# Optimization experiments

Hardware: AMD Instinct MI355X
Metric: run time of the kernel (lower is better)

The kernel has to match this reference:

```python
import jax, jax.numpy as jnp
import numpy as np
from jax import lax


def _gauss1d(size, sigma):
    k = np.arange(size, dtype=np.float32) - (size - 1) / 2.0
    k = np.exp(-0.5 * (k / sigma) ** 2)
    return k / k.sum()


def _make_kernel(scale, sigma):
    # make_odd
    kx, ky, kz = [s + 1 if s % 2 == 0 else s for s in scale]
    kH = _gauss1d(kx, sigma)
    kW = _gauss1d(ky, sigma)
    kD = _gauss1d(kz, sigma)
    kern = kH[:, None, None] * kW[None, :, None] * kD[None, None, :]  # (kx, ky, kz)
    kern = np.transpose(kern, (2, 0, 1))  # permute(2,0,1) -> (kz, kx, ky)
    return jnp.asarray(kern, dtype=jnp.float32)


def setup_inputs() -> dict:
    key = jax.random.key(0)
    x = jax.random.normal(key, (2, 1, 256, 256, 256), dtype=jnp.float32)
    kernel0 = _make_kernel((2, 2, 2), 1.0)  # (3,3,3)
    kernel1 = _make_kernel((4, 4, 4), 1.0)  # (5,5,5)
    return {"x": x, "kernel0": kernel0, "kernel1": kernel1}


def _blur_down(x, kernel, stride):
    # replicate pad by k//2 per spatial dim, then depthwise (C=1) conv3d.
    pad = [(0, 0), (0, 0)] + [(k // 2, k // 2) for k in kernel.shape]
    xp = jnp.pad(x, pad, mode='edge')
    # strided VALID conv == full blur followed by [::s] slicing (output ceil(H/s))
    return lax.conv_general_dilated(
        xp, kernel[None, None].astype(x.dtype),
        window_strides=stride, padding='VALID',
        dimension_numbers=('NCDHW', 'OIDHW', 'NCDHW'))


def reference(x, kernel0, kernel1):
    d1 = _blur_down(x, kernel0, (2, 2, 2))  # (2,1,128,128,128)
    d2 = _blur_down(x, kernel1, (4, 4, 4))  # (2,1,64,64,64)
    return (x, d1, d2)
```

## Files before the change

kernel.cpp:

```cpp
#include <hip/hip_runtime.h>

#define S_IN 256
#define S_D1 128
#define S_D2 64
#define IN_PER_BATCH (S_IN * S_IN * S_IN)
#define D1_PER_BATCH (S_D1 * S_D1 * S_D1)
#define D2_PER_BATCH (S_D2 * S_D2 * S_D2)
#define X_ELEMS (2 * IN_PER_BATCH)
#define D1_ELEMS (2 * D1_PER_BATCH)
#define D2_ELEMS (2 * D2_PER_BATCH)

#define TD 8
#define TH 8
#define TW 32
#define LZ 12
#define LY 12
#define LX 40
#define NV (LZ * LY * (LX / 4))
#define LDS_ELEMS (LZ * LY * LX)

__global__ __launch_bounds__(256) void fused_pyramid(
    const float* __restrict__ x, const float* __restrict__ k0,
    const float* __restrict__ k1, float* __restrict__ out0,
    float* __restrict__ out1, float* __restrict__ out2)
{
    __shared__ float ls[LDS_ELEMS];
    __shared__ float kw0[27];
    __shared__ float kw1[125];

    const int tid = threadIdx.x;
    if (tid < 27) kw0[tid] = k0[tid];
    else if (tid >= 32 && tid < 157) kw1[tid - 32] = k1[tid - 32];

    const int bx = blockIdx.x;
    const int lin = (bx & 7) * 2048 + (bx >> 3);
    const int wt = lin & 7;
    const int hy = (lin >> 3) & 31;
    const int dz = (lin >> 8) & 31;
    const int n  = lin >> 13;

    const int x0 = wt * TW;
    const int y0 = hy * TH;
    const int z0 = dz * TD;

    const float* xb = x + (size_t)n * IN_PER_BATCH;
    float* ob0 = out0 + (size_t)n * IN_PER_BATCH;
    float* ob1 = out1 + (size_t)n * D1_PER_BATCH;
    float* ob2 = out2 + (size_t)n * D2_PER_BATCH;

    float4 vals[6];
#pragma unroll
    for (int i = 0; i < 6; ++i) {
        int v = tid + (i << 8);
        if (v < NV) {
            int row = v / 10;
            int j   = v - row * 10;
            int lz  = row / LY;
            int ly  = row - lz * LY;
            int gz = z0 + lz - 2; gz = gz < 0 ? 0 : (gz > 255 ? 255 : gz);
            int gy = y0 + ly - 2; gy = gy < 0 ? 0 : (gy > 255 ? 255 : gy);
            const float* rp = xb + ((size_t)gz * S_IN + gy) * S_IN;
            int gx = x0 - 4 + (j << 2);
            if (gx >= 0 && gx <= S_IN - 4) {
                vals[i] = *reinterpret_cast<const float4*>(rp + gx);
            } else {
                float s = rp[gx < 0 ? 0 : (S_IN - 1)];
                vals[i] = make_float4(s, s, s, s);
            }
        }
    }
#pragma unroll
    for (int i = 0; i < 6; ++i) {
        int v = tid + (i << 8);
        if (v < NV) {
            int row = v / 10;
            int j   = v - row * 10;
            int lz  = row / LY;
            int ly  = row - lz * LY;
            *reinterpret_cast<float4*>(&ls[(lz * LY + ly) * LX + (j << 2)]) = vals[i];
            if ((unsigned)(lz - 2) < 8u && (unsigned)(ly - 2) < 8u &&
                (unsigned)(j - 1) < 8u) {
                int gz = z0 + lz - 2, gy = y0 + ly - 2, gx = x0 - 4 + (j << 2);
                *reinterpret_cast<float4*>(
                    &ob0[((size_t)gz * S_IN + gy) * S_IN + gx]) = vals[i];
            }
        }
    }
    __syncthreads();

    {
        const int ox = tid & 15;
        const int oy = (tid >> 4) & 3;
        const int oz = tid >> 6;
        float acc = 0.0f;
#pragma unroll
        for (int a = 0; a < 3; ++a) {
            int lz = 2 * oz + 1 + a;
#pragma unroll
            for (int b = 0; b < 3; ++b) {
                int ly = 2 * oy + 1 + b;
                const float* base = &ls[(lz * LY + ly) * LX + 2 * ox + 2];
                float2 v0 = *reinterpret_cast<const float2*>(base);
                float2 v1 = *reinterpret_cast<const float2*>(base + 2);
                const float* kr = &kw0[(a * 3 + b) * 3];
                acc = fmaf(kr[0], v0.y, acc);
                acc = fmaf(kr[1], v1.x, acc);
                acc = fmaf(kr[2], v1.y, acc);
            }
        }
        int d = 4 * dz + oz, h = 4 * hy + oy, w = 16 * wt + ox;
        ob1[((size_t)d * S_D1 + h) * S_D1 + w] = acc;
    }

    {
        const int q = tid & 7;
        const int o = tid >> 3;
        const int ox = o & 7;
        const int oy = (o >> 3) & 1;
        const int oz = o >> 4;
        float acc = 0.0f;
#pragma unroll
        for (int m = 0; m < 4; ++m) {
            int r = q + (m << 3);
            if (r < 25) {
                int a = r / 5, b = r - 5 * a;
                int lz = 4 * oz + a, ly = 4 * oy + b;
                const float* base = &ls[(lz * LY + ly) * LX + 4 * ox];
                float4 A = *reinterpret_cast<const float4*>(base);
                float4 B = *reinterpret_cast<const float4*>(base + 4);
                const float* kr = &kw1[r * 5];
                acc = fmaf(kr[0], A.z, acc);
                acc = fmaf(kr[1], A.w, acc);
                acc = fmaf(kr[2], B.x, acc);
                acc = fmaf(kr[3], B.y, acc);
                acc = fmaf(kr[4], B.z, acc);
            }
        }
        acc += __shfl_xor(acc, 1);
        acc += __shfl_xor(acc, 2);
        acc += __shfl_xor(acc, 4);
        if (q == 0) {
            int d = 2 * dz + oz, h = 2 * hy + oy, w = 8 * wt + ox;
            ob2[((size_t)d * S_D2 + h) * S_D2 + w] = acc;
        }
    }
}

extern "C" void kernel_launch(void* const* d_in, const int* in_sizes, int n_in,
                              void* d_out, int out_size, void* d_ws, size_t ws_size,
                              hipStream_t stream) {
    const float* x  = (const float*)d_in[0];
    const float* k0 = (const float*)d_in[1];
    const float* k1 = (const float*)d_in[2];

    float* out0 = (float*)d_out;
    float* out1 = out0 + X_ELEMS;
    float* out2 = out1 + D1_ELEMS;

    const int blocks = 8 * 32 * 32 * 2;
    fused_pyramid<<<blocks, 256, 0, stream>>>(x, k0, k1, out0, out1, out2);
}
```

Baseline: 303.7 us.

## Persist blocks over 8 z-tiles with double-buffered direct global-to-LDS loads

The kernel becomes persistent: 2048 blocks each process 8 z-tiles in sequence. Halo tiles are fetched with global_load_lds straight into one of two LDS buffers, so the next tile's load overlaps the current tile's convolution. The x copy to out0 is now read back from LDS. Left-edge replicate padding is patched with an extra scalar load and LDS write, which adds syncs for wt==0 blocks. LDS use doubles, which may lower occupancy, and the per-block loop serializes work that was spread across more blocks.

```diff
diff --git a/kernel.cpp b/kernel.cpp
--- a/kernel.cpp
+++ b/kernel.cpp
@@ -1,148 +1,187 @@
 #include <hip/hip_runtime.h>
 
 #define S_IN 256
-#define S_D1 128
-#define S_D2 64
 #define IN_PER_BATCH (S_IN * S_IN * S_IN)
-#define D1_PER_BATCH (S_D1 * S_D1 * S_D1)
-#define D2_PER_BATCH (S_D2 * S_D2 * S_D2)
+#define D1_PER_BATCH (128 * 128 * 128)
+#define D2_PER_BATCH (64 * 64 * 64)
 #define X_ELEMS (2 * IN_PER_BATCH)
 #define D1_ELEMS (2 * D1_PER_BATCH)
 #define D2_ELEMS (2 * D2_PER_BATCH)
 
-#define TD 8
-#define TH 8
-#define TW 32
-#define LZ 12
-#define LY 12
-#define LX 40
-#define NV (LZ * LY * (LX / 4))
-#define LDS_ELEMS (LZ * LY * LX)
+#define LXR 40
+#define NROW 144
+#define BUFV 1536
+#define BUFF (BUFV * 4)
+#define TPB 8
+#define NBLK 2048
+
+__device__ __forceinline__ void gload_lds16(const float* g, float* l) {
+    __builtin_amdgcn_global_load_lds(
+        (const __attribute__((address_space(1))) void*)g,
+        (__attribute__((address_space(3))) void*)l, 16, 0, 0);
+}
 
 __global__ __launch_bounds__(256) void fused_pyramid(
     const float* __restrict__ x, const float* __restrict__ k0,
     const float* __restrict__ k1, float* __restrict__ out0,
     float* __restrict__ out1, float* __restrict__ out2)
 {
-    __shared__ float ls[LDS_ELEMS];
-    __shared__ float kw0[27];
-    __shared__ float kw1[125];
+    __shared__ float ls[2 * BUFF];
+    __shared__ float kw0[9][4];
+    __shared__ float kw1[25][8];
 
     const int tid = threadIdx.x;
-    if (tid < 27) kw0[tid] = k0[tid];
-    else if (tid >= 32 && tid < 157) kw1[tid - 32] = k1[tid - 32];
-
-    const int bx = blockIdx.x;
-    const int lin = (bx & 7) * 2048 + (bx >> 3);
-    const int wt = lin & 7;
-    const int hy = (lin >> 3) & 31;
-    const int dz = (lin >> 8) & 31;
-    const int n  = lin >> 13;
-
-    const int x0 = wt * TW;
-    const int y0 = hy * TH;
-    const int z0 = dz * TD;
-
-    const float* xb = x + (size_t)n * IN_PER_BATCH;
-    float* ob0 = out0 + (size_t)n * IN_PER_BATCH;
-    float* ob1 = out1 + (size_t)n * D1_PER_BATCH;
-    float* ob2 = out2 + (size_t)n * D2_PER_BATCH;
-
-    float4 vals[6];
+    if (tid < 27) kw0[tid / 3][tid % 3] = k0[tid];
+    else if (tid >= 32 && tid < 157) {
+        int t = tid - 32;
+        kw1[t / 5][t % 5] = k1[t];
+    }
+
+    const int bid  = blockIdx.x;
+    const int wt   = bid & 7;
+    const int hy   = (bid >> 3) & 31;
+    const int dzn0 = bid >> 8;
+    const int x0 = wt << 5;
+    const int y0 = hy << 3;
+    const bool edge = (wt == 0);
+
+    int gcol[6];
+    int lzo[6];
 #pragma unroll
     for (int i = 0; i < 6; ++i) {
         int v = tid + (i << 8);
-        if (v < NV) {
-            int row = v / 10;
-            int j   = v - row * 10;
-            int lz  = row / LY;
-            int ly  = row - lz * LY;
-            int gz = z0 + lz - 2; gz = gz < 0 ? 0 : (gz > 255 ? 255 : gz);
-            int gy = y0 + ly - 2; gy = gy < 0 ? 0 : (gy > 255 ? 255 : gy);
-            const float* rp = xb + ((size_t)gz * S_IN + gy) * S_IN;
-            int gx = x0 - 4 + (j << 2);
-            if (gx >= 0 && gx <= S_IN - 4) {
-                vals[i] = *reinterpret_cast<const float4*>(rp + gx);
-            } else {
-                float s = rp[gx < 0 ? 0 : (S_IN - 1)];
-                vals[i] = make_float4(s, s, s, s);
+        int row = v / 10;
+        int j = v - row * 10;
+        int lz = row / 12;
+        int ly = row - lz * 12;
+        int gy = y0 + ly - 2; gy = gy < 0 ? 0 : (gy > 255 ? 255 : gy);
+        int gx = x0 - 4 + (j << 2); gx = gx < 0 ? 0 : (gx > 252 ? 252 : gx);
+        gcol[i] = (gy << 8) + gx;
+        lzo[i] = lz - 2;
+    }
+
+    const bool pact = edge && (tid < NROW);
+    int plz = 0, ply = 0, pgy = 0;
+    if (pact) {
+        plz = tid / 12;
+        ply = tid - plz * 12;
+        int gy = y0 + ply - 2; pgy = gy < 0 ? 0 : (gy > 255 ? 255 : gy);
+    }
+    float pv = 0.0f;
+
+    auto issue_dma = [&](int dzn, int buf) {
+        const int z0 = (dzn & 31) << 3;
+        const float* xb = x + (size_t)(dzn >> 5) * IN_PER_BATCH;
+        float* lb = ls + buf * BUFF + (tid << 2);
+#pragma unroll
+        for (int i = 0; i < 6; ++i) {
+            int gz = z0 + lzo[i]; gz = gz < 0 ? 0 : (gz > 255 ? 255 : gz);
+            gload_lds16(xb + (((size_t)gz << 16) + gcol[i]), lb + (size_t)i * 1024);
+        }
+    };
+    auto patch_load = [&](int dzn) {
+        if (pact) {
+            int z0 = (dzn & 31) << 3;
+            int gz = z0 + plz - 2; gz = gz < 0 ? 0 : (gz > 255 ? 255 : gz);
+            pv = x[(size_t)(dzn >> 5) * IN_PER_BATCH + ((size_t)gz << 16) + (pgy << 8)];
+        }
+    };
+    auto patch_write = [&](int buf) {
+        if (pact) {
+            *reinterpret_cast<float2*>(
+                &ls[buf * BUFF + (plz * 12 + ply) * LXR + 2]) = make_float2(pv, pv);
+        }
+    };
+
+    auto compute = [&](int dzn, int buf) {
+        const int dz = dzn & 31;
+        const int n  = dzn >> 5;
+        const float* B = ls + buf * BUFF;
+
+        {
+            float* ob0 = out0 + (size_t)n * IN_PER_BATCH
+                       + (((size_t)dz << 3) << 16) + (y0 << 8) + x0;
+#pragma unroll
+            for (int k = 0; k < 2; ++k) {
+                int v = tid + (k << 8);
+                int jj = v & 7;
+                int rowc = v >> 3;
+                int lzc = rowc >> 3, lyc = rowc & 7;
+                float4 val = *reinterpret_cast<const float4*>(
+                    &B[((lzc + 2) * 12 + (lyc + 2)) * LXR + 4 + (jj << 2)]);
+                *reinterpret_cast<float4*>(
+                    &ob0[((size_t)lzc << 16) + (lyc << 8) + (jj << 2)]) = val;
             }
         }
-    }
-#pragma unroll
-    for (int i = 0; i < 6; ++i) {
-        int v = tid + (i << 8);
-        if (v < NV) {
-            int row = v / 10;
-            int j   = v - row * 10;
-            int lz  = row / LY;
-            int ly  = row - lz * LY;
-            *reinterpret_cast<float4*>(&ls[(lz * LY + ly) * LX + (j << 2)]) = vals[i];
-            if ((unsigned)(lz - 2) < 8u && (unsigned)(ly - 2) < 8u &&
-                (unsigned)(j - 1) < 8u) {
-                int gz = z0 + lz - 2, gy = y0 + ly - 2, gx = x0 - 4 + (j << 2);
-                *reinterpret_cast<float4*>(
-                    &ob0[((size_t)gz * S_IN + gy) * S_IN + gx]) = vals[i];
+
+        {
+            const int ox = tid & 15, oy = (tid >> 4) & 3, oz = tid >> 6;
+            const float* base = B + ((2 * oz + 1) * 12 + (2 * oy + 1)) * LXR + 2 * ox + 2;
+            float acc = 0.0f;
+#pragma unroll
+            for (int a = 0; a < 3; ++a)
+#pragma unroll
+                for (int b = 0; b < 3; ++b) {
+                    const float* lr = base + (a * 12 + b) * LXR;
+                    float2 v0 = *reinterpret_cast<const float2*>(lr);
+                    float2 v1 = *reinterpret_cast<const float2*>(lr + 2);
+                    float4 kr = *reinterpret_cast<const float4*>(&kw0[a * 3 + b][0]);
+                    acc = fmaf(kr.x, v0.y, acc);
+                    acc = fmaf(kr.y, v1.x, acc);
+                    acc = fmaf(kr.z, v1.y, acc);
+                }
+            float* ob1 = out1 + (size_t)n * D1_PER_BATCH
+                       + (((size_t)dz << 2) << 14) + ((hy << 2) << 7) + (wt << 4);
+            ob1[(oz << 14) + (oy << 7) + ox] = acc;
+        }
+
+        {
+            const int q = tid & 7;
+            const int o = tid >> 3;
+            const int ox = o & 7, oy = (o >> 3) & 1, oz = o >> 4;
+            float acc = 0.0f;
+#pragma unroll
+            for (int m = 0; m < 4; ++m) {
+                int r = q + (m << 3);
+                if (r < 25) {
+                    int a = r / 5, b = r - 5 * a;
+                    const float* lr = B + ((4 * oz + a) * 12 + (4 * oy + b)) * LXR + 4 * ox;
+                    float4 A4 = *reinterpret_cast<const float4*>(lr);
+                    float4 B4 = *reinterpret_cast<const float4*>(lr + 4);
+                    float4 kr = *reinterpret_cast<const float4*>(&kw1[r][0]);
+                    float k4 = kw1[r][4];
+                    acc = fmaf(kr.x, A4.z, acc);
+                    acc = fmaf(kr.y, A4.w, acc);
+                    acc = fmaf(kr.z, B4.x, acc);
+                    acc = fmaf(kr.w, B4.y, acc);
+                    acc = fmaf(k4,   B4.z, acc);
+                }
             }
-        }
-    }
+            acc += __shfl_xor(acc, 1);
+            acc += __shfl_xor(acc, 2);
+            acc += __shfl_xor(acc, 4);
+            if (q == 0) {
+                float* ob2 = out2 + (size_t)n * D2_PER_BATCH
+                           + (((size_t)dz << 1) << 12) + ((hy << 1) << 6) + (wt << 3);
+                ob2[(oz << 12) + (oy << 6) + ox] = acc;
+            }
+        }
+    };
+
+    issue_dma(dzn0, 0);
+    if (edge) patch_load(dzn0);
     __syncthreads();
-
-    {
-        const int ox = tid & 15;
-        const int oy = (tid >> 4) & 3;
-        const int oz = tid >> 6;
-        float acc = 0.0f;
-#pragma unroll
-        for (int a = 0; a < 3; ++a) {
-            int lz = 2 * oz + 1 + a;
-#pragma unroll
-            for (int b = 0; b < 3; ++b) {
-                int ly = 2 * oy + 1 + b;
-                const float* base = &ls[(lz * LY + ly) * LX + 2 * ox + 2];
-                float2 v0 = *reinterpret_cast<const float2*>(base);
-                float2 v1 = *reinterpret_cast<const float2*>(base + 2);
-                const float* kr = &kw0[(a * 3 + b) * 3];
-                acc = fmaf(kr[0], v0.y, acc);
-                acc = fmaf(kr[1], v1.x, acc);
-                acc = fmaf(kr[2], v1.y, acc);
-            }
-        }
-        int d = 4 * dz + oz, h = 4 * hy + oy, w = 16 * wt + ox;
-        ob1[((size_t)d * S_D1 + h) * S_D1 + w] = acc;
-    }
-
-    {
-        const int q = tid & 7;
-        const int o = tid >> 3;
-        const int ox = o & 7;
-        const int oy = (o >> 3) & 1;
-        const int oz = o >> 4;
-        float acc = 0.0f;
-#pragma unroll
-        for (int m = 0; m < 4; ++m) {
-            int r = q + (m << 3);
-            if (r < 25) {
-                int a = r / 5, b = r - 5 * a;
-                int lz = 4 * oz + a, ly = 4 * oy + b;
-                const float* base = &ls[(lz * LY + ly) * LX + 4 * ox];
-                float4 A = *reinterpret_cast<const float4*>(base);
-                float4 B = *reinterpret_cast<const float4*>(base + 4);
-                const float* kr = &kw1[r * 5];
-                acc = fmaf(kr[0], A.z, acc);
-                acc = fmaf(kr[1], A.w, acc);
-                acc = fmaf(kr[2], B.x, acc);
-                acc = fmaf(kr[3], B.y, acc);
-                acc = fmaf(kr[4], B.z, acc);
-            }
-        }
-        acc += __shfl_xor(acc, 1);
-        acc += __shfl_xor(acc, 2);
-        acc += __shfl_xor(acc, 4);
-        if (q == 0) {
-            int d = 2 * dz + oz, h = 2 * hy + oy, w = 8 * wt + ox;
-            ob2[((size_t)d * S_D2 + h) * S_D2 + w] = acc;
-        }
+    if (edge) { patch_write(0); __syncthreads(); }
+
+    for (int it = 0; it < TPB; ++it) {
+        const int cur = it & 1;
+        if (it + 1 < TPB) {
+            issue_dma(dzn0 + 8 * (it + 1), cur ^ 1);
+            if (edge) patch_load(dzn0 + 8 * (it + 1));
+        }
+        compute(dzn0 + 8 * it, cur);
+        __syncthreads();
+        if (edge && it + 1 < TPB) { patch_write(cur ^ 1); __syncthreads(); }
     }
 }
 
@@ -157,6 +196,5 @@
     float* out1 = out0 + X_ELEMS;
     float* out2 = out1 + D1_ELEMS;
 
-    const int blocks = 8 * 32 * 32 * 2;
-    fused_pyramid<<<blocks, 256, 0, stream>>>(x, k0, k1, out0, out1, out2);
+    fused_pyramid<<<NBLK, 256, 0, stream>>>(x, k0, k1, out0, out1, out2);
 }
```

Result: faster. 296.0 us (-2.5%).
